# Kernel tuning notes

Measured on AMD Instinct MI355X. Metric: run time of the kernel, lower is better.

Reference implementation:

```python
import jax, jax.numpy as jnp
import numpy as np
from jax import lax

INPLANES = 512
PLANES = 512
MID = PLANES // 4  # expansion = 4
G = 4              # patch_groups
EPS = 1e-5


def _conv(x, w, groups, pad):
    return lax.conv_general_dilated(
        x, w, window_strides=(1, 1), padding=[(pad, pad), (pad, pad)],
        dimension_numbers=('NCHW', 'OIHW', 'NCHW'), feature_group_count=groups)


def _bn(x, gamma, beta, mean, var):
    scale = gamma / jnp.sqrt(var + EPS)
    return x * scale[None, :, None, None] + (beta - mean * scale)[None, :, None, None]


def _upmask(mask, c, h, w):
    # [b,g,mh,mw] -> repeat each group over c//g channels (group-major channel order),
    # then nearest-upsample to (h, w) (exact integer repeat, matches F.interpolate nearest)
    b, g, mh, mw = mask.shape
    m = jnp.repeat(mask, c // g, axis=1)
    m = jnp.repeat(m, h // mh, axis=2)
    m = jnp.repeat(m, w // mw, axis=3)
    return m


def setup_inputs() -> dict:
    key = jax.random.key(0)
    ks = jax.random.split(key, 20)
    x = jax.random.normal(ks[0], (16, INPLANES, 56, 56), dtype=jnp.float32)
    mask = jax.random.randint(ks[1], (16, G, 7, 7), 0, 2).astype(jnp.float32)
    s = 0.05
    w1 = jax.random.normal(ks[2], (MID, INPLANES // G, 1, 1), dtype=jnp.float32) * s
    w2 = jax.random.normal(ks[3], (MID, MID // G, 3, 3), dtype=jnp.float32) * s
    w3 = jax.random.normal(ks[4], (PLANES, MID // G, 1, 1), dtype=jnp.float32) * s
    def bnp(k, c):
        k1, k2, k3, k4 = jax.random.split(k, 4)
        return (jax.random.normal(k1, (c,), jnp.float32) * 0.1 + 1.0,  # gamma
                jax.random.normal(k2, (c,), jnp.float32) * 0.1,        # beta
                jax.random.normal(k3, (c,), jnp.float32) * 0.1,        # running mean
                jax.random.uniform(k4, (c,), jnp.float32, 0.5, 1.5))   # running var
    g1, b1, m1, v1 = bnp(ks[5], MID)
    g2, b2, m2, v2 = bnp(ks[6], MID)
    g3, b3, m3, v3 = bnp(ks[7], PLANES)
    return dict(x=x, mask=mask, w1=w1, g1=g1, b1=b1, m1=m1, v1=v1,
                w2=w2, g2=g2, b2=b2, m2=m2, v2=v2,
                w3=w3, g3=g3, b3=b3, m3=m3, v3=v3)


def reference(x, mask, w1, g1, b1, m1, v1, w2, g2, b2, m2, v2, w3, g3, b3, m3, v3):
    b, c, h, w = x.shape
    residual = x
    mask1 = _upmask(mask, c, h, w)           # [b, c, h, w]
    out = x * mask1
    out = jax.nn.relu(_bn(_conv(out, w1, G, 0), g1, b1, m1, v1))  # [b, MID, h, w]
    mask2 = _upmask(mask, out.shape[1], h, w)
    out = out * mask2
    out = jax.nn.relu(_bn(_conv(out, w2, G, 1), g2, b2, m2, v2))
    out = out * mask2
    out = _bn(_conv(out, w3, G, 0), g3, b3, m3, v3)
    out = out + residual
    return jax.nn.relu(out)
```

## Files before the change

### kernel.cpp

```cpp
#include <hip/hip_runtime.h>
#include <stdint.h>

typedef unsigned short U16;
typedef unsigned int   U32;
typedef __attribute__((ext_vector_type(8))) short short8;
typedef __attribute__((ext_vector_type(4))) float floatx4;

#define HW 3136

__device__ __forceinline__ U16 f2b(float f){
    union { float f; unsigned int i; } v; v.f = f;
    unsigned int u = (v.i + 0x7FFFu + ((v.i >> 16) & 1u)) >> 16;
    return (U16)u;
}
__device__ __forceinline__ short8 pack8(const float* p){
    float4 a = *reinterpret_cast<const float4*>(p);
    float4 b = *reinterpret_cast<const float4*>(p + 4);
    short8 r;
    r[0]=(short)f2b(a.x); r[1]=(short)f2b(a.y); r[2]=(short)f2b(a.z); r[3]=(short)f2b(a.w);
    r[4]=(short)f2b(b.x); r[5]=(short)f2b(b.y); r[6]=(short)f2b(b.z); r[7]=(short)f2b(b.w);
    return r;
}

__global__ void k_pre(const float* __restrict__ w2,
                      const float* g1, const float* b1, const float* m1, const float* v1,
                      const float* g2, const float* b2, const float* m2, const float* v2,
                      const float* g3, const float* b3, const float* m3, const float* v3,
                      U16* __restrict__ w2t, float* __restrict__ bn){
  int i = blockIdx.x * 256 + threadIdx.x;
  if (i < 4*9*32*32) {
    int ic  = i & 31;
    int oc  = (i >> 5) & 31;
    int gt  = i >> 10;
    int g_  = gt / 9, tap = gt % 9;
    w2t[i] = f2b(w2[((g_*32 + oc)*32 + ic)*9 + tap]);
  } else {
    int j = i - 4*9*32*32;
    if (j >= 768) return;
    const float *gp, *bp, *mp, *vp; int c, so, sho;
    if (j < 128)      { c = j;       gp=g1; bp=b1; mp=m1; vp=v1; so = 0;   sho = 128;  }
    else if (j < 256) { c = j - 128; gp=g2; bp=b2; mp=m2; vp=v2; so = 256; sho = 384;  }
    else              { c = j - 256; gp=g3; bp=b3; mp=m3; vp=v3; so = 512; sho = 1024; }
    float s = gp[c] / sqrtf(vp[c] + 1e-5f);
    bn[so + c]  = s;
    bn[sho + c] = bp[c] - mp[c] * s;
  }
}

__global__ __launch_bounds__(256) void k_conv1(const float* __restrict__ x,
        const float* __restrict__ mask, const float* __restrict__ w1,
        const float* __restrict__ bn, U16* __restrict__ t1){
  const int t = threadIdx.x;
  const int lane = t & 63, wave = t >> 6;
  const int quad = lane >> 4, l15 = lane & 15;
  const int b = blockIdx.z, g = blockIdx.y, mh = blockIdx.x;
  const int h0 = mh*8, wbase = wave*112;
  __shared__ float mk[7];
  __shared__ __align__(16) U16 xs[32*456];
  if (t < 7) mk[t] = mask[((b*4 + g)*7 + mh)*7 + t];
  const float* xg = x + (size_t)(b*512 + g*128)*HW + h0*56;
  U16* t1g = t1 + (size_t)(b*128 + g*32)*HW + h0*56;

  const float* wg = w1 + (size_t)(g*32)*128;
  short8 afr[2][4];
  #pragma unroll
  for (int oct = 0; oct < 2; ++oct)
    #pragma unroll
    for (int ks = 0; ks < 4; ++ks)
      afr[oct][ks] = pack8(wg + (oct*16 + l15)*128 + ks*32 + quad*8);

  floatx4 acc[2][7] = {};
  #pragma unroll
  for (int ch = 0; ch < 4; ++ch){
    __syncthreads();
    #pragma unroll
    for (int k = 0; k < 14; ++k){
      int idx = k*256 + t;
      int ic = idx / 112, f = idx - ic*112;
      int px = f*4;
      float4 v = *reinterpret_cast<const float4*>(xg + (size_t)(ch*32 + ic)*HW + px);
      float m = mk[(px % 56) >> 3];
      U32 lo = (U32)f2b(v.x*m) | ((U32)f2b(v.y*m) << 16);
      U32 hi = (U32)f2b(v.z*m) | ((U32)f2b(v.w*m) << 16);
      *reinterpret_cast<uint2*>(&xs[ic*456 + px]) = make_uint2(lo, hi);
    }
    __syncthreads();
    #pragma unroll
    for (int pxt = 0; pxt < 7; ++pxt){
      short8 bfr;
      #pragma unroll
      for (int j = 0; j < 8; ++j)
        bfr[j] = (short)xs[(quad*8 + j)*456 + wbase + pxt*16 + l15];
      acc[0][pxt] = __builtin_amdgcn_mfma_f32_16x16x32_bf16(afr[0][ch], bfr, acc[0][pxt], 0,0,0);
      acc[1][pxt] = __builtin_amdgcn_mfma_f32_16x16x32_bf16(afr[1][ch], bfr, acc[1][pxt], 0,0,0);
    }
  }
  #pragma unroll
  for (int oct = 0; oct < 2; ++oct)
    #pragma unroll
    for (int reg = 0; reg < 4; ++reg){
      int oc = oct*16 + quad*4 + reg;
      float sc = bn[g*32 + oc], sh = bn[128 + g*32 + oc];
      #pragma unroll
      for (int pxt = 0; pxt < 7; ++pxt){
        int px = wbase + pxt*16 + l15;
        float y = fmaxf(sc*acc[oct][pxt][reg] + sh, 0.0f) * mk[(px % 56) >> 3];
        t1g[(size_t)oc*HW + px] = f2b(y);
      }
    }
}

__global__ __launch_bounds__(256) void k_conv2(const U16* __restrict__ t1,
        const float* __restrict__ mask, const U16* __restrict__ w2t,
        const float* __restrict__ bn, U16* __restrict__ t2){
  const int t = threadIdx.x;
  const int lane = t & 63, wave = t >> 6;
  const int quad = lane >> 4, l15 = lane & 15;
  const int b = blockIdx.z, g = blockIdx.y, mh = blockIdx.x;
  const int h0 = mh*8;
  __shared__ float mk[7];
  __shared__ __align__(16) U16 s[32*720];
  if (t < 7) mk[t] = mask[((b*4 + g)*7 + mh)*7 + t];
  #pragma unroll
  for (int e = t; e < 320; e += 256){
    int ic = e / 10, r = e - ic*10;
    s[(ic*10 + r)*72 + 7]  = 0;
    s[(ic*10 + r)*72 + 64] = 0;
  }
  const U16* tg = t1 + (size_t)(b*128 + g*32)*HW;
  #pragma unroll
  for (int k = 0; k < 9; ++k){
    int idx = k*256 + t;
    if (idx < 2240){
      int ic = idx / 70, rem = idx - ic*70;
      int r = rem / 7, seg = rem - r*7;
      int hh = h0 - 1 + r;
      uint4 v = make_uint4(0,0,0,0);
      if (hh >= 0 && hh < 56)
        v = *reinterpret_cast<const uint4*>(tg + (size_t)ic*HW + hh*56 + seg*8);
      *reinterpret_cast<uint4*>(&s[(ic*10 + r)*72 + 8 + seg*8]) = v;
    }
  }
  __syncthreads();
  const U16* wg = w2t + g*9*32*32;
  floatx4 acc[2][7] = {};
  #pragma unroll
  for (int kh = 0; kh < 3; ++kh){
    const int lr = wave*2 + (l15 >> 3) + kh;
    #pragma unroll
    for (int kw = 0; kw < 3; ++kw){
      int tap = kh*3 + kw;
      short8 a0 = *reinterpret_cast<const short8*>(wg + (tap*32 +      l15)*32 + quad*8);
      short8 a1 = *reinterpret_cast<const short8*>(wg + (tap*32 + 16 + l15)*32 + quad*8);
      #pragma unroll
      for (int pxt = 0; pxt < 7; ++pxt){
        int lc = 7 + pxt*8 + (l15 & 7) + kw;
        short8 bfr;
        #pragma unroll
        for (int j = 0; j < 8; ++j)
          bfr[j] = (short)s[((quad*8 + j)*10 + lr)*72 + lc];
        acc[0][pxt] = __builtin_amdgcn_mfma_f32_16x16x32_bf16(a0, bfr, acc[0][pxt], 0,0,0);
        acc[1][pxt] = __builtin_amdgcn_mfma_f32_16x16x32_bf16(a1, bfr, acc[1][pxt], 0,0,0);
      }
    }
  }
  U16* og = t2 + (size_t)(b*128 + g*32)*HW + h0*56;
  const int pr = wave*2 + (l15 >> 3);
  #pragma unroll
  for (int oct = 0; oct < 2; ++oct)
    #pragma unroll
    for (int reg = 0; reg < 4; ++reg){
      int oc = oct*16 + quad*4 + reg;
      float sc = bn[256 + g*32 + oc], sh = bn[384 + g*32 + oc];
      #pragma unroll
      for (int pxt = 0; pxt < 7; ++pxt){
        float y = fmaxf(sc*acc[oct][pxt][reg] + sh, 0.0f) * mk[pxt];
        og[oc*HW + pr*56 + pxt*8 + (l15 & 7)] = f2b(y);
      }
    }
}

__global__ __launch_bounds__(256) void k_conv3(const U16* __restrict__ t2,
        const float* __restrict__ x, const float* __restrict__ w3,
        const float* __restrict__ bn, float* __restrict__ out){
  const int t = threadIdx.x;
  const int lane = t & 63, wave = t >> 6;
  const int quad = lane >> 4, l15 = lane & 15;
  const int b = blockIdx.z, g = blockIdx.y, mh = blockIdx.x;
  const int h0 = mh*8, wbase = wave*112;
  __shared__ __align__(16) U16 xs[32*456];
  const U16* tg = t2 + (size_t)(b*128 + g*32)*HW + h0*56;
  #pragma unroll
  for (int k = 0; k < 7; ++k){
    int idx = k*256 + t;
    int ic = idx / 56, seg = idx - ic*56;
    *reinterpret_cast<uint4*>(&xs[ic*456 + seg*8]) =
        *reinterpret_cast<const uint4*>(tg + (size_t)ic*HW + seg*8);
  }
  __syncthreads();
  short8 bfr[7];
  #pragma unroll
  for (int pxt = 0; pxt < 7; ++pxt)
    #pragma unroll
    for (int j = 0; j < 8; ++j)
      bfr[pxt][j] = (short)xs[(quad*8 + j)*456 + wbase + pxt*16 + l15];
  const float* xg = x + (size_t)(b*512 + g*128)*HW + h0*56;
  float* og = out + (size_t)(b*512 + g*128)*HW + h0*56;
  #pragma unroll
  for (int oct = 0; oct < 8; ++oct){
    short8 afr = pack8(w3 + (size_t)(g*128 + oct*16 + l15)*32 + quad*8);
    floatx4 acc[7] = {};
    #pragma unroll
    for (int pxt = 0; pxt < 7; ++pxt)
      acc[pxt] = __builtin_amdgcn_mfma_f32_16x16x32_bf16(afr, bfr[pxt], acc[pxt], 0,0,0);
    #pragma unroll
    for (int reg = 0; reg < 4; ++reg){
      int oc = oct*16 + quad*4 + reg;
      float sc = bn[512 + g*128 + oc], sh = bn[1024 + g*128 + oc];
      #pragma unroll
      for (int pxt = 0; pxt < 7; ++pxt){
        size_t o2 = (size_t)oc*HW + wbase + pxt*16 + l15;
        og[o2] = fmaxf(sc*acc[pxt][reg] + sh + xg[o2], 0.0f);
      }
    }
  }
}

extern "C" void kernel_launch(void* const* d_in, const int* in_sizes, int n_in,
                              void* d_out, int out_size, void* d_ws, size_t ws_size,
                              hipStream_t stream){
  const float* x    = (const float*)d_in[0];
  const float* mask = (const float*)d_in[1];
  const float* w1   = (const float*)d_in[2];
  const float* g1   = (const float*)d_in[3];
  const float* b1   = (const float*)d_in[4];
  const float* m1   = (const float*)d_in[5];
  const float* v1   = (const float*)d_in[6];
  const float* w2   = (const float*)d_in[7];
  const float* g2   = (const float*)d_in[8];
  const float* b2   = (const float*)d_in[9];
  const float* m2   = (const float*)d_in[10];
  const float* v2   = (const float*)d_in[11];
  const float* w3   = (const float*)d_in[12];
  const float* g3   = (const float*)d_in[13];
  const float* b3   = (const float*)d_in[14];
  const float* m3   = (const float*)d_in[15];
  const float* v3   = (const float*)d_in[16];

  char* ws = (char*)d_ws;
  U16*   w2t = (U16*)ws;
  float* bn  = (float*)(ws + 73728);
  U16*   t1  = (U16*)(ws + 79872);
  U16*   t2  = (U16*)(ws + 79872 + 12845056);

  k_pre<<<147, 256, 0, stream>>>(w2, g1,b1,m1,v1, g2,b2,m2,v2, g3,b3,m3,v3, w2t, bn);
  dim3 grid(7, 4, 16);
  k_conv1<<<grid, 256, 0, stream>>>(x, mask, w1, bn, t1);
  k_conv2<<<grid, 256, 0, stream>>>(t1, mask, w2t, bn, t2);
  k_conv3<<<grid, 256, 0, stream>>>(t2, x, w3, bn, (float*)d_out);
}
```

Baseline: 289.8 us.

## Split output-channel tiles across more waves per block in all three convs

Each conv kernel now launches more waves per block (512 threads for conv1/conv2, 1024 for conv3), with each wave owning a subset of output-channel tiles instead of looping over all of them. The grid is only 448 blocks, so the intent is more waves resident per CU to hide memory latency and spread MFMA work. The cost is fewer MFMAs per wave to amortize the shared-memory B-fragment loads, since the same LDS data is now read by more waves, and heavier register and LDS pressure per block.

```diff
diff --git a/kernel.cpp b/kernel.cpp
--- a/kernel.cpp
+++ b/kernel.cpp
@@ -47,14 +47,15 @@
   }
 }
 
-__global__ __launch_bounds__(256) void k_conv1(const float* __restrict__ x,
+__global__ __launch_bounds__(512) void k_conv1(const float* __restrict__ x,
         const float* __restrict__ mask, const float* __restrict__ w1,
         const float* __restrict__ bn, U16* __restrict__ t1){
   const int t = threadIdx.x;
   const int lane = t & 63, wave = t >> 6;
   const int quad = lane >> 4, l15 = lane & 15;
+  const int oct = wave & 1, pxq = wave >> 1;
   const int b = blockIdx.z, g = blockIdx.y, mh = blockIdx.x;
-  const int h0 = mh*8, wbase = wave*112;
+  const int h0 = mh*8, wbase = pxq*112;
   __shared__ float mk[7];
   __shared__ __align__(16) U16 xs[32*456];
   if (t < 7) mk[t] = mask[((b*4 + g)*7 + mh)*7 + t];
@@ -62,20 +63,18 @@
   U16* t1g = t1 + (size_t)(b*128 + g*32)*HW + h0*56;
 
   const float* wg = w1 + (size_t)(g*32)*128;
-  short8 afr[2][4];
-  #pragma unroll
-  for (int oct = 0; oct < 2; ++oct)
-    #pragma unroll
-    for (int ks = 0; ks < 4; ++ks)
-      afr[oct][ks] = pack8(wg + (oct*16 + l15)*128 + ks*32 + quad*8);
-
-  floatx4 acc[2][7] = {};
+  short8 afr[4];
+  #pragma unroll
+  for (int ks = 0; ks < 4; ++ks)
+    afr[ks] = pack8(wg + (oct*16 + l15)*128 + ks*32 + quad*8);
+
+  floatx4 acc[7] = {};
   #pragma unroll
   for (int ch = 0; ch < 4; ++ch){
     __syncthreads();
     #pragma unroll
-    for (int k = 0; k < 14; ++k){
-      int idx = k*256 + t;
+    for (int k = 0; k < 7; ++k){
+      int idx = k*512 + t;
       int ic = idx / 112, f = idx - ic*112;
       int px = f*4;
       float4 v = *reinterpret_cast<const float4*>(xg + (size_t)(ch*32 + ic)*HW + px);
@@ -91,46 +90,43 @@
       #pragma unroll
       for (int j = 0; j < 8; ++j)
         bfr[j] = (short)xs[(quad*8 + j)*456 + wbase + pxt*16 + l15];
-      acc[0][pxt] = __builtin_amdgcn_mfma_f32_16x16x32_bf16(afr[0][ch], bfr, acc[0][pxt], 0,0,0);
-      acc[1][pxt] = __builtin_amdgcn_mfma_f32_16x16x32_bf16(afr[1][ch], bfr, acc[1][pxt], 0,0,0);
-    }
-  }
-  #pragma unroll
-  for (int oct = 0; oct < 2; ++oct)
-    #pragma unroll
-    for (int reg = 0; reg < 4; ++reg){
-      int oc = oct*16 + quad*4 + reg;
-      float sc = bn[g*32 + oc], sh = bn[128 + g*32 + oc];
-      #pragma unroll
-      for (int pxt = 0; pxt < 7; ++pxt){
-        int px = wbase + pxt*16 + l15;
-        float y = fmaxf(sc*acc[oct][pxt][reg] + sh, 0.0f) * mk[(px % 56) >> 3];
-        t1g[(size_t)oc*HW + px] = f2b(y);
-      }
-    }
-}
-
-__global__ __launch_bounds__(256) void k_conv2(const U16* __restrict__ t1,
+      acc[pxt] = __builtin_amdgcn_mfma_f32_16x16x32_bf16(afr[ch], bfr, acc[pxt], 0,0,0);
+    }
+  }
+  #pragma unroll
+  for (int reg = 0; reg < 4; ++reg){
+    int oc = oct*16 + quad*4 + reg;
+    float sc = bn[g*32 + oc], sh = bn[128 + g*32 + oc];
+    #pragma unroll
+    for (int pxt = 0; pxt < 7; ++pxt){
+      int px = wbase + pxt*16 + l15;
+      float y = fmaxf(sc*acc[pxt][reg] + sh, 0.0f) * mk[(px % 56) >> 3];
+      t1g[(size_t)oc*HW + px] = f2b(y);
+    }
+  }
+}
+
+__global__ __launch_bounds__(512) void k_conv2(const U16* __restrict__ t1,
         const float* __restrict__ mask, const U16* __restrict__ w2t,
         const float* __restrict__ bn, U16* __restrict__ t2){
   const int t = threadIdx.x;
   const int lane = t & 63, wave = t >> 6;
   const int quad = lane >> 4, l15 = lane & 15;
+  const int oct = wave & 1, rq = wave >> 1;
   const int b = blockIdx.z, g = blockIdx.y, mh = blockIdx.x;
   const int h0 = mh*8;
   __shared__ float mk[7];
   __shared__ __align__(16) U16 s[32*720];
   if (t < 7) mk[t] = mask[((b*4 + g)*7 + mh)*7 + t];
-  #pragma unroll
-  for (int e = t; e < 320; e += 256){
-    int ic = e / 10, r = e - ic*10;
+  if (t < 320){
+    int ic = t / 10, r = t - ic*10;
     s[(ic*10 + r)*72 + 7]  = 0;
     s[(ic*10 + r)*72 + 64] = 0;
   }
   const U16* tg = t1 + (size_t)(b*128 + g*32)*HW;
   #pragma unroll
-  for (int k = 0; k < 9; ++k){
-    int idx = k*256 + t;
+  for (int k = 0; k < 5; ++k){
+    int idx = k*512 + t;
     if (idx < 2240){
       int ic = idx / 70, rem = idx - ic*70;
       int r = rem / 7, seg = rem - r*7;
@@ -143,15 +139,14 @@
   }
   __syncthreads();
   const U16* wg = w2t + g*9*32*32;
-  floatx4 acc[2][7] = {};
+  floatx4 acc[7] = {};
   #pragma unroll
   for (int kh = 0; kh < 3; ++kh){
-    const int lr = wave*2 + (l15 >> 3) + kh;
+    const int lr = rq*2 + (l15 >> 3) + kh;
     #pragma unroll
     for (int kw = 0; kw < 3; ++kw){
       int tap = kh*3 + kw;
-      short8 a0 = *reinterpret_cast<const short8*>(wg + (tap*32 +      l15)*32 + quad*8);
-      short8 a1 = *reinterpret_cast<const short8*>(wg + (tap*32 + 16 + l15)*32 + quad*8);
+      short8 a0 = *reinterpret_cast<const short8*>(wg + (tap*32 + oct*16 + l15)*32 + quad*8);
       #pragma unroll
       for (int pxt = 0; pxt < 7; ++pxt){
         int lc = 7 + pxt*8 + (l15 & 7) + kw;
@@ -159,43 +154,43 @@
         #pragma unroll
         for (int j = 0; j < 8; ++j)
           bfr[j] = (short)s[((quad*8 + j)*10 + lr)*72 + lc];
-        acc[0][pxt] = __builtin_amdgcn_mfma_f32_16x16x32_bf16(a0, bfr, acc[0][pxt], 0,0,0);
-        acc[1][pxt] = __builtin_amdgcn_mfma_f32_16x16x32_bf16(a1, bfr, acc[1][pxt], 0,0,0);
+        acc[pxt] = __builtin_amdgcn_mfma_f32_16x16x32_bf16(a0, bfr, acc[pxt], 0,0,0);
       }
     }
   }
   U16* og = t2 + (size_t)(b*128 + g*32)*HW + h0*56;
-  const int pr = wave*2 + (l15 >> 3);
-  #pragma unroll
-  for (int oct = 0; oct < 2; ++oct)
-    #pragma unroll
-    for (int reg = 0; reg < 4; ++reg){
-      int oc = oct*16 + quad*4 + reg;
-      float sc = bn[256 + g*32 + oc], sh = bn[384 + g*32 + oc];
-      #pragma unroll
-      for (int pxt = 0; pxt < 7; ++pxt){
-        float y = fmaxf(sc*acc[oct][pxt][reg] + sh, 0.0f) * mk[pxt];
-        og[oc*HW + pr*56 + pxt*8 + (l15 & 7)] = f2b(y);
-      }
-    }
-}
-
-__global__ __launch_bounds__(256) void k_conv3(const U16* __restrict__ t2,
+  const int pr = rq*2 + (l15 >> 3);
+  #pragma unroll
+  for (int reg = 0; reg < 4; ++reg){
+    int oc = oct*16 + quad*4 + reg;
+    float sc = bn[256 + g*32 + oc], sh = bn[384 + g*32 + oc];
+    #pragma unroll
+    for (int pxt = 0; pxt < 7; ++pxt){
+      float y = fmaxf(sc*acc[pxt][reg] + sh, 0.0f) * mk[pxt];
+      og[oc*HW + pr*56 + pxt*8 + (l15 & 7)] = f2b(y);
+    }
+  }
+}
+
+__global__ __launch_bounds__(1024) void k_conv3(const U16* __restrict__ t2,
         const float* __restrict__ x, const float* __restrict__ w3,
         const float* __restrict__ bn, float* __restrict__ out){
   const int t = threadIdx.x;
   const int lane = t & 63, wave = t >> 6;
   const int quad = lane >> 4, l15 = lane & 15;
+  const int pxq = wave & 3, ocp = wave >> 2;
   const int b = blockIdx.z, g = blockIdx.y, mh = blockIdx.x;
-  const int h0 = mh*8, wbase = wave*112;
+  const int h0 = mh*8, wbase = pxq*112;
   __shared__ __align__(16) U16 xs[32*456];
   const U16* tg = t2 + (size_t)(b*128 + g*32)*HW + h0*56;
   #pragma unroll
-  for (int k = 0; k < 7; ++k){
-    int idx = k*256 + t;
-    int ic = idx / 56, seg = idx - ic*56;
-    *reinterpret_cast<uint4*>(&xs[ic*456 + seg*8]) =
-        *reinterpret_cast<const uint4*>(tg + (size_t)ic*HW + seg*8);
+  for (int k = 0; k < 2; ++k){
+    int idx = k*1024 + t;
+    if (idx < 1792){
+      int ic = idx / 56, seg = idx - ic*56;
+      *reinterpret_cast<uint4*>(&xs[ic*456 + seg*8]) =
+          *reinterpret_cast<const uint4*>(tg + (size_t)ic*HW + seg*8);
+    }
   }
   __syncthreads();
   short8 bfr[7];
@@ -207,7 +202,8 @@
   const float* xg = x + (size_t)(b*512 + g*128)*HW + h0*56;
   float* og = out + (size_t)(b*512 + g*128)*HW + h0*56;
   #pragma unroll
-  for (int oct = 0; oct < 8; ++oct){
+  for (int o2 = 0; o2 < 2; ++o2){
+    const int oct = ocp*2 + o2;
     short8 afr = pack8(w3 + (size_t)(g*128 + oct*16 + l15)*32 + quad*8);
     floatx4 acc[7] = {};
     #pragma unroll
@@ -219,8 +215,8 @@
       float sc = bn[512 + g*128 + oc], sh = bn[1024 + g*128 + oc];
       #pragma unroll
       for (int pxt = 0; pxt < 7; ++pxt){
-        size_t o2 = (size_t)oc*HW + wbase + pxt*16 + l15;
-        og[o2] = fmaxf(sc*acc[pxt][reg] + sh + xg[o2], 0.0f);
+        size_t o2i = (size_t)oc*HW + wbase + pxt*16 + l15;
+        og[o2i] = fmaxf(sc*acc[pxt][reg] + sh + xg[o2i], 0.0f);
       }
     }
   }
@@ -255,7 +251,7 @@
 
   k_pre<<<147, 256, 0, stream>>>(w2, g1,b1,m1,v1, g2,b2,m2,v2, g3,b3,m3,v3, w2t, bn);
   dim3 grid(7, 4, 16);
-  k_conv1<<<grid, 256, 0, stream>>>(x, mask, w1, bn, t1);
-  k_conv2<<<grid, 256, 0, stream>>>(t1, mask, w2t, bn, t2);
-  k_conv3<<<grid, 256, 0, stream>>>(t2, x, w3, bn, (float*)d_out);
-}
+  k_conv1<<<grid, 512, 0, stream>>>(x, mask, w1, bn, t1);
+  k_conv2<<<grid, 512, 0, stream>>>(t1, mask, w2t, bn, t2);
+  k_conv3<<<grid, 1024, 0, stream>>>(t2, x, w3, bn, (float*)d_out);
+}
```

Result: faster. 270.7 us (-6.6%).

## Switch intermediates to pixel-major channel-last layout and drop LDS staging

Applied to the files above, without the earlier changes.

The t1/t2 intermediates move from channel-planar to pixel-major layout with 32 channels contiguous per pixel. All three conv kernels now load MFMA operands straight from global memory instead of staging through shared memory. The grid grows to 49 blocks of 64 pixels per (group, batch), and conv1 drops to 128 threads. This removes LDS traffic, barriers and the halo setup, and should raise occupancy, but conv1 now does strided scalar fp32 loads from x and conv2 re-reads overlapping neighbourhoods through cache for every tap.

```diff
diff --git a/kernel.cpp b/kernel.cpp
--- a/kernel.cpp
+++ b/kernel.cpp
@@ -47,20 +47,25 @@
   }
 }
 
-__global__ __launch_bounds__(256) void k_conv1(const float* __restrict__ x,
+__global__ __launch_bounds__(128) void k_conv1(const float* __restrict__ x,
         const float* __restrict__ mask, const float* __restrict__ w1,
         const float* __restrict__ bn, U16* __restrict__ t1){
   const int t = threadIdx.x;
   const int lane = t & 63, wave = t >> 6;
   const int quad = lane >> 4, l15 = lane & 15;
-  const int b = blockIdx.z, g = blockIdx.y, mh = blockIdx.x;
-  const int h0 = mh*8, wbase = wave*112;
-  __shared__ float mk[7];
-  __shared__ __align__(16) U16 xs[32*456];
-  if (t < 7) mk[t] = mask[((b*4 + g)*7 + mh)*7 + t];
-  const float* xg = x + (size_t)(b*512 + g*128)*HW + h0*56;
-  U16* t1g = t1 + (size_t)(b*128 + g*32)*HW + h0*56;
-
+  const int b = blockIdx.z, g = blockIdx.y;
+  const int px0 = blockIdx.x*64 + wave*32;
+  const float* xg = x + (size_t)(b*512 + g*128)*HW;
+  U16* t1g = t1 + (size_t)(b*4 + g)*HW*32;
+
+  int pxl[2]; float mfr[2];
+  #pragma unroll
+  for (int pxt = 0; pxt < 2; ++pxt){
+    int px = px0 + pxt*16 + l15;
+    pxl[pxt] = px;
+    int h = px / 56, w = px - h*56;
+    mfr[pxt] = mask[((b*4 + g)*7 + (h>>3))*7 + (w>>3)];
+  }
   const float* wg = w1 + (size_t)(g*32)*128;
   short8 afr[2][4];
   #pragma unroll
@@ -69,45 +74,36 @@
     for (int ks = 0; ks < 4; ++ks)
       afr[oct][ks] = pack8(wg + (oct*16 + l15)*128 + ks*32 + quad*8);
 
-  floatx4 acc[2][7] = {};
+  floatx4 acc[2][2] = {};
   #pragma unroll
   for (int ch = 0; ch < 4; ++ch){
-    __syncthreads();
-    #pragma unroll
-    for (int k = 0; k < 14; ++k){
-      int idx = k*256 + t;
-      int ic = idx / 112, f = idx - ic*112;
-      int px = f*4;
-      float4 v = *reinterpret_cast<const float4*>(xg + (size_t)(ch*32 + ic)*HW + px);
-      float m = mk[(px % 56) >> 3];
-      U32 lo = (U32)f2b(v.x*m) | ((U32)f2b(v.y*m) << 16);
-      U32 hi = (U32)f2b(v.z*m) | ((U32)f2b(v.w*m) << 16);
-      *reinterpret_cast<uint2*>(&xs[ic*456 + px]) = make_uint2(lo, hi);
-    }
-    __syncthreads();
-    #pragma unroll
-    for (int pxt = 0; pxt < 7; ++pxt){
+    #pragma unroll
+    for (int pxt = 0; pxt < 2; ++pxt){
+      const float* bp = xg + (size_t)(ch*32 + quad*8)*HW + pxl[pxt];
+      float m = mfr[pxt];
       short8 bfr;
       #pragma unroll
       for (int j = 0; j < 8; ++j)
-        bfr[j] = (short)xs[(quad*8 + j)*456 + wbase + pxt*16 + l15];
+        bfr[j] = (short)f2b(bp[(size_t)j*HW] * m);
       acc[0][pxt] = __builtin_amdgcn_mfma_f32_16x16x32_bf16(afr[0][ch], bfr, acc[0][pxt], 0,0,0);
       acc[1][pxt] = __builtin_amdgcn_mfma_f32_16x16x32_bf16(afr[1][ch], bfr, acc[1][pxt], 0,0,0);
     }
   }
   #pragma unroll
-  for (int oct = 0; oct < 2; ++oct)
-    #pragma unroll
-    for (int reg = 0; reg < 4; ++reg){
-      int oc = oct*16 + quad*4 + reg;
-      float sc = bn[g*32 + oc], sh = bn[128 + g*32 + oc];
-      #pragma unroll
-      for (int pxt = 0; pxt < 7; ++pxt){
-        int px = wbase + pxt*16 + l15;
-        float y = fmaxf(sc*acc[oct][pxt][reg] + sh, 0.0f) * mk[(px % 56) >> 3];
-        t1g[(size_t)oc*HW + px] = f2b(y);
-      }
-    }
+  for (int oct = 0; oct < 2; ++oct){
+    const float* scp = bn + g*32 + oct*16 + quad*4;
+    const float* shp = scp + 128;
+    #pragma unroll
+    for (int pxt = 0; pxt < 2; ++pxt){
+      float m = mfr[pxt];
+      U16 y[4];
+      #pragma unroll
+      for (int reg = 0; reg < 4; ++reg)
+        y[reg] = f2b(fmaxf(scp[reg]*acc[oct][pxt][reg] + shp[reg], 0.0f) * m);
+      uint2 pk = make_uint2((U32)y[0] | ((U32)y[1]<<16), (U32)y[2] | ((U32)y[3]<<16));
+      *reinterpret_cast<uint2*>(t1g + (size_t)pxl[pxt]*32 + oct*16 + quad*4) = pk;
+    }
+  }
 }
 
 __global__ __launch_bounds__(256) void k_conv2(const U16* __restrict__ t1,
@@ -116,68 +112,52 @@
   const int t = threadIdx.x;
   const int lane = t & 63, wave = t >> 6;
   const int quad = lane >> 4, l15 = lane & 15;
-  const int b = blockIdx.z, g = blockIdx.y, mh = blockIdx.x;
-  const int h0 = mh*8;
-  __shared__ float mk[7];
-  __shared__ __align__(16) U16 s[32*720];
-  if (t < 7) mk[t] = mask[((b*4 + g)*7 + mh)*7 + t];
-  #pragma unroll
-  for (int e = t; e < 320; e += 256){
-    int ic = e / 10, r = e - ic*10;
-    s[(ic*10 + r)*72 + 7]  = 0;
-    s[(ic*10 + r)*72 + 64] = 0;
-  }
-  const U16* tg = t1 + (size_t)(b*128 + g*32)*HW;
-  #pragma unroll
-  for (int k = 0; k < 9; ++k){
-    int idx = k*256 + t;
-    if (idx < 2240){
-      int ic = idx / 70, rem = idx - ic*70;
-      int r = rem / 7, seg = rem - r*7;
-      int hh = h0 - 1 + r;
-      uint4 v = make_uint4(0,0,0,0);
-      if (hh >= 0 && hh < 56)
-        v = *reinterpret_cast<const uint4*>(tg + (size_t)ic*HW + hh*56 + seg*8);
-      *reinterpret_cast<uint4*>(&s[(ic*10 + r)*72 + 8 + seg*8]) = v;
-    }
-  }
-  __syncthreads();
+  const int oct = wave & 1;
+  const int b = blockIdx.z, g = blockIdx.y;
+  const int px0 = blockIdx.x*64 + (wave>>1)*32;
+  const U16* tg = t1 + (size_t)(b*4 + g)*HW*32;
+  U16*       og = t2 + (size_t)(b*4 + g)*HW*32;
+
+  int pxl[2], hh[2], wwc[2]; float mfr[2];
+  #pragma unroll
+  for (int pxt = 0; pxt < 2; ++pxt){
+    int px = px0 + pxt*16 + l15;
+    pxl[pxt] = px;
+    int h = px / 56, w = px - h*56;
+    hh[pxt] = h; wwc[pxt] = w;
+    mfr[pxt] = mask[((b*4 + g)*7 + (h>>3))*7 + (w>>3)];
+  }
   const U16* wg = w2t + g*9*32*32;
-  floatx4 acc[2][7] = {};
-  #pragma unroll
-  for (int kh = 0; kh < 3; ++kh){
-    const int lr = wave*2 + (l15 >> 3) + kh;
+  floatx4 acc[2] = {};
+  #pragma unroll
+  for (int kh = 0; kh < 3; ++kh)
     #pragma unroll
     for (int kw = 0; kw < 3; ++kw){
       int tap = kh*3 + kw;
-      short8 a0 = *reinterpret_cast<const short8*>(wg + (tap*32 +      l15)*32 + quad*8);
-      short8 a1 = *reinterpret_cast<const short8*>(wg + (tap*32 + 16 + l15)*32 + quad*8);
-      #pragma unroll
-      for (int pxt = 0; pxt < 7; ++pxt){
-        int lc = 7 + pxt*8 + (l15 & 7) + kw;
+      short8 a = *reinterpret_cast<const short8*>(wg + (tap*32 + oct*16 + l15)*32 + quad*8);
+      #pragma unroll
+      for (int pxt = 0; pxt < 2; ++pxt){
+        int r = hh[pxt] + kh - 1, c = wwc[pxt] + kw - 1;
         short8 bfr;
         #pragma unroll
-        for (int j = 0; j < 8; ++j)
-          bfr[j] = (short)s[((quad*8 + j)*10 + lr)*72 + lc];
-        acc[0][pxt] = __builtin_amdgcn_mfma_f32_16x16x32_bf16(a0, bfr, acc[0][pxt], 0,0,0);
-        acc[1][pxt] = __builtin_amdgcn_mfma_f32_16x16x32_bf16(a1, bfr, acc[1][pxt], 0,0,0);
+        for (int j = 0; j < 8; ++j) bfr[j] = 0;
+        if ((unsigned)r < 56u && (unsigned)c < 56u)
+          bfr = *reinterpret_cast<const short8*>(tg + (size_t)(r*56 + c)*32 + quad*8);
+        acc[pxt] = __builtin_amdgcn_mfma_f32_16x16x32_bf16(a, bfr, acc[pxt], 0,0,0);
       }
     }
-  }
-  U16* og = t2 + (size_t)(b*128 + g*32)*HW + h0*56;
-  const int pr = wave*2 + (l15 >> 3);
-  #pragma unroll
-  for (int oct = 0; oct < 2; ++oct)
-    #pragma unroll
-    for (int reg = 0; reg < 4; ++reg){
-      int oc = oct*16 + quad*4 + reg;
-      float sc = bn[256 + g*32 + oc], sh = bn[384 + g*32 + oc];
-      #pragma unroll
-      for (int pxt = 0; pxt < 7; ++pxt){
-        float y = fmaxf(sc*acc[oct][pxt][reg] + sh, 0.0f) * mk[pxt];
-        og[oc*HW + pr*56 + pxt*8 + (l15 & 7)] = f2b(y);
-      }
-    }
+  const float* scp = bn + 256 + g*32 + oct*16 + quad*4;
+  const float* shp = bn + 384 + g*32 + oct*16 + quad*4;
+  #pragma unroll
+  for (int pxt = 0; pxt < 2; ++pxt){
+    float m = mfr[pxt];
+    U16 y[4];
+    #pragma unroll
+    for (int reg = 0; reg < 4; ++reg)
+      y[reg] = f2b(fmaxf(scp[reg]*acc[pxt][reg] + shp[reg], 0.0f) * m);
+    uint2 pk = make_uint2((U32)y[0] | ((U32)y[1]<<16), (U32)y[2] | ((U32)y[3]<<16));
+    *reinterpret_cast<uint2*>(og + (size_t)pxl[pxt]*32 + oct*16 + quad*4) = pk;
+  }
 }
 
 __global__ __launch_bounds__(256) void k_conv3(const U16* __restrict__ t2,
@@ -186,40 +166,38 @@
   const int t = threadIdx.x;
   const int lane = t & 63, wave = t >> 6;
   const int quad = lane >> 4, l15 = lane & 15;
-  const int b = blockIdx.z, g = blockIdx.y, mh = blockIdx.x;
-  const int h0 = mh*8, wbase = wave*112;
-  __shared__ __align__(16) U16 xs[32*456];
-  const U16* tg = t2 + (size_t)(b*128 + g*32)*HW + h0*56;
-  #pragma unroll
-  for (int k = 0; k < 7; ++k){
-    int idx = k*256 + t;
-    int ic = idx / 56, seg = idx - ic*56;
-    *reinterpret_cast<uint4*>(&xs[ic*456 + seg*8]) =
-        *reinterpret_cast<const uint4*>(tg + (size_t)ic*HW + seg*8);
-  }
-  __syncthreads();
-  short8 bfr[7];
-  #pragma unroll
-  for (int pxt = 0; pxt < 7; ++pxt)
-    #pragma unroll
-    for (int j = 0; j < 8; ++j)
-      bfr[pxt][j] = (short)xs[(quad*8 + j)*456 + wbase + pxt*16 + l15];
-  const float* xg = x + (size_t)(b*512 + g*128)*HW + h0*56;
-  float* og = out + (size_t)(b*512 + g*128)*HW + h0*56;
-  #pragma unroll
-  for (int oct = 0; oct < 8; ++oct){
+  const int oh = wave & 1;
+  const int b = blockIdx.z, g = blockIdx.y;
+  const int px0 = blockIdx.x*64 + (wave>>1)*32;
+  const U16* tg = t2 + (size_t)(b*4 + g)*HW*32;
+  const float* xg = x + (size_t)(b*512 + g*128)*HW;
+  float*       og = out + (size_t)(b*512 + g*128)*HW;
+
+  int pxl[2];
+  short8 bfr[2];
+  #pragma unroll
+  for (int pxt = 0; pxt < 2; ++pxt){
+    int px = px0 + pxt*16 + l15;
+    pxl[pxt] = px;
+    bfr[pxt] = *reinterpret_cast<const short8*>(tg + (size_t)px*32 + quad*8);
+  }
+  #pragma unroll
+  for (int o4 = 0; o4 < 4; ++o4){
+    int oct = oh*4 + o4;
     short8 afr = pack8(w3 + (size_t)(g*128 + oct*16 + l15)*32 + quad*8);
-    floatx4 acc[7] = {};
-    #pragma unroll
-    for (int pxt = 0; pxt < 7; ++pxt)
+    floatx4 acc[2] = {};
+    #pragma unroll
+    for (int pxt = 0; pxt < 2; ++pxt)
       acc[pxt] = __builtin_amdgcn_mfma_f32_16x16x32_bf16(afr, bfr[pxt], acc[pxt], 0,0,0);
+    const float* scp = bn + 512 + g*128 + oct*16 + quad*4;
+    const float* shp = bn + 1024 + g*128 + oct*16 + quad*4;
     #pragma unroll
     for (int reg = 0; reg < 4; ++reg){
       int oc = oct*16 + quad*4 + reg;
-      float sc = bn[512 + g*128 + oc], sh = bn[1024 + g*128 + oc];
-      #pragma unroll
-      for (int pxt = 0; pxt < 7; ++pxt){
-        size_t o2 = (size_t)oc*HW + wbase + pxt*16 + l15;
+      float sc = scp[reg], sh = shp[reg];
+      #pragma unroll
+      for (int pxt = 0; pxt < 2; ++pxt){
+        size_t o2 = (size_t)oc*HW + pxl[pxt];
         og[o2] = fmaxf(sc*acc[pxt][reg] + sh + xg[o2], 0.0f);
       }
     }
@@ -254,8 +232,8 @@
   U16*   t2  = (U16*)(ws + 79872 + 12845056);
 
   k_pre<<<147, 256, 0, stream>>>(w2, g1,b1,m1,v1, g2,b2,m2,v2, g3,b3,m3,v3, w2t, bn);
-  dim3 grid(7, 4, 16);
-  k_conv1<<<grid, 256, 0, stream>>>(x, mask, w1, bn, t1);
+  dim3 grid(49, 4, 16);
+  k_conv1<<<grid, 128, 0, stream>>>(x, mask, w1, bn, t1);
   k_conv2<<<grid, 256, 0, stream>>>(t1, mask, w2t, bn, t2);
   k_conv3<<<grid, 256, 0, stream>>>(t2, x, w3, bn, (float*)d_out);
 }
```

Result: faster. 274.2 us (-5.4%).
